# Performance work log

Hardware: AMD Instinct MI355X
Metric: run time of the kernel (lower is better)

The kernel has to match this reference:

```python
import jax, jax.numpy as jnp
import numpy as np

D_MODEL = 1024
NHEAD = 16
HEAD_DIM = D_MODEL // NHEAD


def setup_inputs() -> dict:
    key = jax.random.key(0)
    ks = jax.random.split(key, 9)
    s = 0.02
    x = jax.random.normal(ks[0], (2, 2048, D_MODEL), dtype=jnp.float32)
    Wq = jax.random.normal(ks[1], (D_MODEL, D_MODEL), dtype=jnp.float32) * s
    bq = jnp.zeros((D_MODEL,), jnp.float32)
    Wk = jax.random.normal(ks[2], (D_MODEL, D_MODEL), dtype=jnp.float32) * s
    bk = jnp.zeros((D_MODEL,), jnp.float32)
    Wv = jax.random.normal(ks[3], (D_MODEL, D_MODEL), dtype=jnp.float32) * s
    bv = jnp.zeros((D_MODEL,), jnp.float32)
    Wo = jax.random.normal(ks[4], (D_MODEL, D_MODEL), dtype=jnp.float32) * s
    bo = jnp.zeros((D_MODEL,), jnp.float32)
    return {"x": x, "Wq": Wq, "bq": bq, "Wk": Wk, "bk": bk,
            "Wv": Wv, "bv": bv, "Wo": Wo, "bo": bo}


def _rope(x, sin, cos):
    # x: [B, L, H, Dh]; rotate-half as in the torch module
    half = x.shape[-1] // 2
    x1, x2 = x[..., :half], x[..., half:]
    rotated = jnp.concatenate([-x2, x1], axis=-1)
    return x * cos + rotated * sin


def reference(x, Wq, bq, Wk, bk, Wv, bv, Wo, bo):
    B, L, D = x.shape
    H, Dh = NHEAD, HEAD_DIM
    q = (x @ Wq.T + bq).reshape(B, L, H, Dh)
    k = (x @ Wk.T + bk).reshape(B, L, H, Dh)
    v = (x @ Wv.T + bv).reshape(B, L, H, Dh)

    inv_freq = 1.0 / (10000.0 ** (jnp.arange(0, Dh, 2, dtype=jnp.float32) / Dh))
    t = jnp.arange(L, dtype=jnp.float32)
    freqs = jnp.einsum('i,j->ij', t, inv_freq)          # [L, Dh/2]
    emb = jnp.concatenate([freqs, freqs], axis=-1)      # [L, Dh]
    cos = jnp.cos(emb)[None, :, None, :]
    sin = jnp.sin(emb)[None, :, None, :]

    q = _rope(q, sin, cos)
    k = _rope(k, sin, cos)

    # [B, H, L, L]
    scores = jnp.einsum('bqhd,bkhd->bhqk', q, k) / jnp.sqrt(jnp.float32(Dh))
    attn = jax.nn.softmax(scores, axis=-1)
    # dropout in eval mode = identity (p given as 0.0)
    out = jnp.einsum('bhqk,bkhd->bqhd', attn, v).reshape(B, L, D)
    return out @ Wo.T + bo
```

## Files before the change

### kernel.cpp

```cpp
#include <hip/hip_runtime.h>
#include <math.h>

#define D_MODEL 1024
#define NHEAD 16
#define HEAD_DIM 64
#define L_SEQ 2048
#define BATCH 2
#define M_ROWS 4096
#define SC_Q 0.18033688011112042f

typedef __attribute__((ext_vector_type(8))) short short8;
typedef __attribute__((ext_vector_type(4))) float floatx4;
typedef __attribute__((ext_vector_type(2))) __fp16 half2_t;
typedef __attribute__((ext_vector_type(4))) __fp16 half4_t;

#if __has_builtin(__builtin_amdgcn_exp2f)
#define EXP2F(x) __builtin_amdgcn_exp2f(x)
#else
#define EXP2F(x) exp2f(x)
#endif

__device__ inline unsigned f2bf_u(float x) {
    unsigned u = __float_as_uint(x);
    return (u + 0x7fffu + ((u >> 16) & 1u)) >> 16;
}

__device__ inline void gl_lds16(const void* g, void* l) {
    __builtin_amdgcn_global_load_lds((const __attribute__((address_space(1))) void*)g,
                                     (__attribute__((address_space(3))) void*)l, 16, 0, 0);
}

__global__ __launch_bounds__(256) void cvt_all(
    const float* __restrict__ x,  const float* __restrict__ wq,
    const float* __restrict__ wk, const float* __restrict__ wv,
    const float* __restrict__ wo,
    unsigned short* __restrict__ xb,  unsigned short* __restrict__ wqb,
    unsigned short* __restrict__ wkb, unsigned short* __restrict__ wvb,
    unsigned short* __restrict__ wob, float* __restrict__ rt) {
    if (blockIdx.y == 5) {
        for (int idx = blockIdx.x * 256 + threadIdx.x; idx < L_SEQ * 16;
             idx += gridDim.x * 256) {
            int l = idx >> 4, f = idx & 15;
            float if0 = (float)pow(10000.0, -(double)f / 32.0);
            float if1 = (float)pow(10000.0, -(double)(f + 16) / 32.0);
            float s0, c0, s1, c1;
            sincosf((float)l * if0, &s0, &c0);
            sincosf((float)l * if1, &s1, &c1);
            float4 v = {c0, c1, s0, s1};
            *(float4*)(rt + (size_t)idx * 4) = v;
        }
        return;
    }
    const float* s; unsigned short* d; int n;
    switch (blockIdx.y) {
        case 0:  s = x;  d = xb;  n = M_ROWS * D_MODEL; break;
        case 1:  s = wq; d = wqb; n = D_MODEL * D_MODEL; break;
        case 2:  s = wk; d = wkb; n = D_MODEL * D_MODEL; break;
        case 3:  s = wv; d = wvb; n = D_MODEL * D_MODEL; break;
        default: s = wo; d = wob; n = D_MODEL * D_MODEL; break;
    }
    int stride = gridDim.x * 256 * 4;
    for (int i = (blockIdx.x * 256 + threadIdx.x) * 4; i < n; i += stride) {
        float4 v = *(const float4*)(s + i);
        ushort4 o;
        o.x = (unsigned short)f2bf_u(v.x);
        o.y = (unsigned short)f2bf_u(v.y);
        o.z = (unsigned short)f2bf_u(v.z);
        o.w = (unsigned short)f2bf_u(v.w);
        *(ushort4*)(d + i) = o;
    }
}

__global__ __launch_bounds__(256) void gemm_qkv(
    const unsigned short* __restrict__ xb,
    const unsigned short* __restrict__ wqb, const unsigned short* __restrict__ wkb,
    const unsigned short* __restrict__ wvb,
    const float* __restrict__ bq, const float* __restrict__ bk,
    const float* __restrict__ bv, const float* __restrict__ rt,
    unsigned short* __restrict__ qo, unsigned short* __restrict__ ko,
    unsigned short* __restrict__ vo) {
    __shared__ __align__(16) unsigned short As[128 * 32];
    __shared__ __align__(16) unsigned short Bs[128 * 32];

    const int K = D_MODEL;
    const int tid = threadIdx.x;
    const int lane = tid & 63;
    const int w = tid >> 6;
    const int wm = (w & 1) * 64;
    const int wn = (w >> 1) * 64;
    const int m0 = blockIdx.x * 128;
    const int n0 = blockIdx.y * 128;

    const unsigned short* Wsel; const float* bsel;
    unsigned short* osel; int mode; float oscale;
    if (blockIdx.z == 0)      { Wsel = wqb; bsel = bq; osel = qo; mode = 1; oscale = SC_Q; }
    else if (blockIdx.z == 1) { Wsel = wkb; bsel = bk; osel = ko; mode = 1; oscale = 1.0f; }
    else                      { Wsel = wvb; bsel = bv; osel = vo; mode = 2; oscale = 1.0f; }

    floatx4 acc[4][4];
#pragma unroll
    for (int i = 0; i < 4; ++i)
#pragma unroll
        for (int j = 0; j < 4; ++j) acc[i][j] = (floatx4){0.f, 0.f, 0.f, 0.f};

    const int sr = lane >> 2;
    const int ss = lane & 3;
    const unsigned short* Ag = xb + (size_t)m0 * K;
    const unsigned short* Bg = Wsel + (size_t)n0 * K;

    for (int k0 = 0; k0 < K; k0 += 32) {
        __syncthreads();
#pragma unroll
        for (int t = 0; t < 2; ++t) {
            int R0 = t * 64 + w * 16;
            int r = R0 + sr;
            int c = ss ^ ((r >> 1) & 3);
            gl_lds16(Ag + (size_t)r * K + k0 + c * 8, (void*)(As + R0 * 32));
            gl_lds16(Bg + (size_t)r * K + k0 + c * 8, (void*)(Bs + R0 * 32));
        }
        __syncthreads();

        short8 af[4], bf[4];
#pragma unroll
        for (int mt = 0; mt < 4; ++mt) {
            int ar = wm + mt * 16 + (lane & 15);
            int slot = (lane >> 4) ^ ((ar >> 1) & 3);
            af[mt] = *(const short8*)(As + ar * 32 + slot * 8);
        }
#pragma unroll
        for (int nt = 0; nt < 4; ++nt) {
            int br = wn + nt * 16 + (lane & 15);
            int slot = (lane >> 4) ^ ((br >> 1) & 3);
            bf[nt] = *(const short8*)(Bs + br * 32 + slot * 8);
        }
#pragma unroll
        for (int mt = 0; mt < 4; ++mt)
#pragma unroll
            for (int nt = 0; nt < 4; ++nt)
                acc[mt][nt] = __builtin_amdgcn_mfma_f32_16x16x32_bf16(
                    af[mt], bf[nt], acc[mt][nt], 0, 0, 0);
    }

#pragma unroll
    for (int nt = 0; nt < 4; ++nt) {
        float bn = bsel[n0 + wn + nt * 16 + (lane & 15)];
#pragma unroll
        for (int mt = 0; mt < 4; ++mt)
#pragma unroll
            for (int i = 0; i < 4; ++i) acc[mt][nt][i] += bn;
    }

    const int h = (n0 + wn) >> 6;

    if (mode == 1) {
#pragma unroll
        for (int mt = 0; mt < 4; ++mt)
#pragma unroll
            for (int i = 0; i < 4; ++i) {
                int m = m0 + wm + mt * 16 + (lane >> 4) * 4 + i;
                int b = m >> 11, l = m & (L_SEQ - 1);
                float4 tc = *(const float4*)(rt + ((size_t)(l * 16 + (lane & 15)) << 2));
#pragma unroll
                for (int nt = 0; nt < 4; ++nt) {
                    int dh = nt * 16 + (lane & 15);
                    float partner = acc[mt][nt ^ 2][i];
                    float rot = (nt < 2) ? -partner : partner;
                    float c = (nt & 1) ? tc.y : tc.x;
                    float s = (nt & 1) ? tc.w : tc.z;
                    float val = (acc[mt][nt][i] * c + rot * s) * oscale;
                    size_t idx = (((size_t)(b * NHEAD + h)) * L_SEQ + l) * HEAD_DIM + dh;
                    osel[idx] = (unsigned short)f2bf_u(val);
                }
            }
    } else {
#pragma unroll
        for (int mt = 0; mt < 4; ++mt)
#pragma unroll
            for (int ih = 0; ih < 4; ih += 2) {
                int m = m0 + wm + mt * 16 + (lane >> 4) * 4 + ih;
                int b = m >> 11, l = m & (L_SEQ - 1);
#pragma unroll
                for (int nt = 0; nt < 4; ++nt) {
                    int dh = nt * 16 + (lane & 15);
                    union { half2_t h; unsigned u; } cv;
                    cv.h = __builtin_amdgcn_cvt_pkrtz(acc[mt][nt][ih], acc[mt][nt][ih + 1]);
                    size_t idx = (((size_t)(b * NHEAD + h)) * HEAD_DIM + dh) * L_SEQ + l;
                    *(unsigned*)(vo + idx) = cv.u;
                }
            }
    }
}

__global__ __launch_bounds__(256) void gemm_out(
    const unsigned short* __restrict__ A, const unsigned short* __restrict__ Wb,
    const float* __restrict__ bias, float* __restrict__ out) {
    __shared__ __align__(16) unsigned short As[64 * 32];
    __shared__ __align__(16) unsigned short Bs[128 * 32];

    const int K = D_MODEL;
    const int tid = threadIdx.x;
    const int lane = tid & 63;
    const int w = tid >> 6;
    const int wm = (w & 1) * 32;
    const int wn = (w >> 1) * 64;
    const int m0 = blockIdx.x * 64;
    const int n0 = blockIdx.y * 128;

    floatx4 acc[2][4];
#pragma unroll
    for (int i = 0; i < 2; ++i)
#pragma unroll
        for (int j = 0; j < 4; ++j) acc[i][j] = (floatx4){0.f, 0.f, 0.f, 0.f};

    const int sr = lane >> 2;
    const int ss = lane & 3;
    const unsigned short* Ag = A + (size_t)m0 * K;
    const unsigned short* Bg = Wb + (size_t)n0 * K;

    for (int k0 = 0; k0 < K; k0 += 32) {
        __syncthreads();
        {
            int r = w * 16 + sr;
            int c = ss ^ ((r >> 1) & 3);
            gl_lds16(Ag + (size_t)r * K + k0 + c * 8, (void*)(As + (w * 16) * 32));
        }
#pragma unroll
        for (int t = 0; t < 2; ++t) {
            int R0 = t * 64 + w * 16;
            int r = R0 + sr;
            int c = ss ^ ((r >> 1) & 3);
            gl_lds16(Bg + (size_t)r * K + k0 + c * 8, (void*)(Bs + R0 * 32));
        }
        __syncthreads();

        short8 af[2], bf[4];
#pragma unroll
        for (int mt = 0; mt < 2; ++mt) {
            int ar = wm + mt * 16 + (lane & 15);
            int slot = (lane >> 4) ^ ((ar >> 1) & 3);
            af[mt] = *(const short8*)(As + ar * 32 + slot * 8);
        }
#pragma unroll
        for (int nt = 0; nt < 4; ++nt) {
            int br = wn + nt * 16 + (lane & 15);
            int slot = (lane >> 4) ^ ((br >> 1) & 3);
            bf[nt] = *(const short8*)(Bs + br * 32 + slot * 8);
        }
#pragma unroll
        for (int mt = 0; mt < 2; ++mt)
#pragma unroll
            for (int nt = 0; nt < 4; ++nt)
                acc[mt][nt] = __builtin_amdgcn_mfma_f32_16x16x32_bf16(
                    af[mt], bf[nt], acc[mt][nt], 0, 0, 0);
    }

#pragma unroll
    for (int nt = 0; nt < 4; ++nt) {
        int n = n0 + wn + nt * 16 + (lane & 15);
        float bn = bias[n];
#pragma unroll
        for (int mt = 0; mt < 2; ++mt)
#pragma unroll
            for (int i = 0; i < 4; ++i) {
                int m = m0 + wm + mt * 16 + (lane >> 4) * 4 + i;
                out[(size_t)m * D_MODEL + n] = acc[mt][nt][i] + bn;
            }
    }
}

template <int NZ>
__global__ __launch_bounds__(256, 4) void attn_mfma(
    const unsigned short* __restrict__ q, const unsigned short* __restrict__ k,
    const unsigned short* __restrict__ vt,
    float* __restrict__ opart, float* __restrict__ lpart,
    unsigned short* __restrict__ ao) {
    __shared__ __align__(16) unsigned short Ks[128 * 64];
    __shared__ __align__(16) unsigned short Vs[64 * 128];

    const int tid = threadIdx.x;
    const int lane = tid & 63;
    const int w = tid >> 6;
    const int quad = lane >> 4;
    const int ln = lane & 15;
    const int bh = blockIdx.y;
    const int q0 = blockIdx.x * 128;
    const int z = blockIdx.z;
    const int kvbase = z * (L_SEQ / NZ);

    const unsigned short* qb = q + (size_t)bh * L_SEQ * HEAD_DIM;
    const unsigned short* kb = k + (size_t)bh * L_SEQ * HEAD_DIM;
    const unsigned short* vb = vt + (size_t)bh * HEAD_DIM * L_SEQ;

    short8 qf[2][2];
#pragma unroll
    for (int ntq = 0; ntq < 2; ++ntq)
#pragma unroll
        for (int ks = 0; ks < 2; ++ks)
            qf[ntq][ks] = *(const short8*)(
                qb + (size_t)(q0 + w * 32 + ntq * 16 + ln) * HEAD_DIM
                + ks * 32 + quad * 8);

    floatx4 o[2][4];
    floatx4 ls[2];
#pragma unroll
    for (int ntq = 0; ntq < 2; ++ntq) {
        ls[ntq] = (floatx4){0.f, 0.f, 0.f, 0.f};
#pragma unroll
        for (int j = 0; j < 4; ++j) o[ntq][j] = (floatx4){0.f, 0.f, 0.f, 0.f};
    }

    half4_t ones;
#pragma unroll
    for (int j = 0; j < 4; ++j) ones[j] = (__fp16)1.0f;

    const int srk = lane >> 3;
    const int ssk = lane & 7;
    const int srv = lane >> 4;
    const int ssv = lane & 15;

    for (int t = 0; t < L_SEQ / (128 * NZ); ++t) {
        int kv0 = kvbase + t * 128;
        __syncthreads();
#pragma unroll
        for (int tt = 0; tt < 4; ++tt) {
            {
                int R0 = tt * 32 + w * 8;
                int r = R0 + srk;
                int c = ssk ^ (r & 7);
                gl_lds16(kb + (size_t)(kv0 + r) * HEAD_DIM + c * 8, (void*)(Ks + R0 * 64));
            }
            {
                int R0 = tt * 16 + w * 4;
                int r = R0 + srv;
                int c = ssv ^ (r & 15);
                gl_lds16(vb + (size_t)r * L_SEQ + kv0 + c * 8, (void*)(Vs + R0 * 128));
            }
        }
        __syncthreads();

#pragma unroll
        for (int mt = 0; mt < 8; ++mt) {
            int ar = mt * 16 + ln;
            short8 kf0 = *(const short8*)(Ks + ar * 64 + ((quad) ^ (ar & 7)) * 8);
            short8 kf1 = *(const short8*)(Ks + ar * 64 + ((4 + quad) ^ (ar & 7)) * 8);

            floatx4 s0 = (floatx4){0.f, 0.f, 0.f, 0.f};
            floatx4 s1 = (floatx4){0.f, 0.f, 0.f, 0.f};
            s0 = __builtin_amdgcn_mfma_f32_16x16x32_bf16(kf0, qf[0][0], s0, 0, 0, 0);
            s0 = __builtin_amdgcn_mfma_f32_16x16x32_bf16(kf1, qf[0][1], s0, 0, 0, 0);
            s1 = __builtin_amdgcn_mfma_f32_16x16x32_bf16(kf0, qf[1][0], s1, 0, 0, 0);
            s1 = __builtin_amdgcn_mfma_f32_16x16x32_bf16(kf1, qf[1][1], s1, 0, 0, 0);

            half4_t vf[4];
#pragma unroll
            for (int ntd = 0; ntd < 4; ++ntd) {
                int row = ntd * 16 + ln;
                int slot = (mt * 2 + (quad >> 1)) ^ ln;
                vf[ntd] = *(const half4_t*)(Vs + row * 128 + slot * 8 + (quad & 1) * 4);
            }

            {
                half2_t lo = __builtin_amdgcn_cvt_pkrtz(EXP2F(s0[0]), EXP2F(s0[1]));
                half2_t hi = __builtin_amdgcn_cvt_pkrtz(EXP2F(s0[2]), EXP2F(s0[3]));
                half4_t af; af.lo = lo; af.hi = hi;
                ls[0] = __builtin_amdgcn_mfma_f32_16x16x16f16(af, ones, ls[0], 0, 0, 0);
#pragma unroll
                for (int ntd = 0; ntd < 4; ++ntd)
                    o[0][ntd] = __builtin_amdgcn_mfma_f32_16x16x16f16(af, vf[ntd], o[0][ntd], 0, 0, 0);
            }
            {
                half2_t lo = __builtin_amdgcn_cvt_pkrtz(EXP2F(s1[0]), EXP2F(s1[1]));
                half2_t hi = __builtin_amdgcn_cvt_pkrtz(EXP2F(s1[2]), EXP2F(s1[3]));
                half4_t af; af.lo = lo; af.hi = hi;
                ls[1] = __builtin_amdgcn_mfma_f32_16x16x16f16(af, ones, ls[1], 0, 0, 0);
#pragma unroll
                for (int ntd = 0; ntd < 4; ++ntd)
                    o[1][ntd] = __builtin_amdgcn_mfma_f32_16x16x16f16(af, vf[ntd], o[1][ntd], 0, 0, 0);
            }
        }
    }

    if (NZ == 1) {
        const int b = bh >> 4, h = bh & (NHEAD - 1);
#pragma unroll
        for (int ntq = 0; ntq < 2; ++ntq)
#pragma unroll
            for (int i = 0; i < 4; ++i) {
                int l = q0 + w * 32 + ntq * 16 + quad * 4 + i;
                float inv = 1.0f / ls[ntq][i];
#pragma unroll
                for (int ntd = 0; ntd < 4; ++ntd) {
                    int dh = ntd * 16 + ln;
                    size_t idx = ((size_t)b * L_SEQ + l) * D_MODEL + h * HEAD_DIM + dh;
                    ao[idx] = (unsigned short)f2bf_u(o[ntq][ntd][i] * inv);
                }
            }
    } else {
        const size_t base = ((size_t)z * (BATCH * NHEAD) + bh) * L_SEQ;
#pragma unroll
        for (int ntq = 0; ntq < 2; ++ntq)
#pragma unroll
            for (int i = 0; i < 4; ++i) {
                int l = q0 + w * 32 + ntq * 16 + quad * 4 + i;
#pragma unroll
                for (int ntd = 0; ntd < 4; ++ntd) {
                    int dh = ntd * 16 + ln;
                    opart[(base + l) * HEAD_DIM + dh] = o[ntq][ntd][i];
                }
            }
        if (ln == 0) {
#pragma unroll
            for (int ntq = 0; ntq < 2; ++ntq)
#pragma unroll
                for (int i = 0; i < 4; ++i) {
                    int l = q0 + w * 32 + ntq * 16 + quad * 4 + i;
                    lpart[base + l] = ls[ntq][i];
                }
        }
    }
}

__global__ __launch_bounds__(256) void attn_combine(
    const float* __restrict__ opart, const float* __restrict__ lpart,
    unsigned short* __restrict__ ao) {
    const size_t R = (size_t)BATCH * NHEAD * L_SEQ;
    int e = blockIdx.x * 256 + threadIdx.x;
    int r = e >> 4;
    int dh0 = (e & 15) * 4;
    float4 a = *(const float4*)(opart + (size_t)r * HEAD_DIM + dh0);
    float4 c = *(const float4*)(opart + (R + r) * HEAD_DIM + dh0);
    float inv = 1.0f / (lpart[r] + lpart[R + r]);
    int bh = r >> 11, l = r & (L_SEQ - 1);
    int b = bh >> 4, h = bh & (NHEAD - 1);
    ushort4 ov;
    ov.x = (unsigned short)f2bf_u((a.x + c.x) * inv);
    ov.y = (unsigned short)f2bf_u((a.y + c.y) * inv);
    ov.z = (unsigned short)f2bf_u((a.z + c.z) * inv);
    ov.w = (unsigned short)f2bf_u((a.w + c.w) * inv);
    *(ushort4*)(ao + ((size_t)b * L_SEQ + l) * D_MODEL + h * HEAD_DIM + dh0) = ov;
}

extern "C" void kernel_launch(void* const* d_in, const int* in_sizes, int n_in,
                              void* d_out, int out_size, void* d_ws, size_t ws_size,
                              hipStream_t stream) {
    const float* x  = (const float*)d_in[0];
    const float* Wq = (const float*)d_in[1];
    const float* bq = (const float*)d_in[2];
    const float* Wk = (const float*)d_in[3];
    const float* bk = (const float*)d_in[4];
    const float* Wv = (const float*)d_in[5];
    const float* bv = (const float*)d_in[6];
    const float* Wo = (const float*)d_in[7];
    const float* bo = (const float*)d_in[8];
    float* outp = (float*)d_out;

    const size_t XE = (size_t)M_ROWS * D_MODEL;
    const size_t WE = (size_t)D_MODEL * D_MODEL;
    unsigned short* wqb = (unsigned short*)d_ws;
    unsigned short* wkb = wqb + WE;
    unsigned short* wvb = wkb + WE;
    unsigned short* wob = wvb + WE;
    unsigned short* qbf = wob + WE;
    unsigned short* kbf = qbf + XE;
    unsigned short* vtb = kbf + XE;
    unsigned short* xb  = vtb + XE;
    unsigned short* aob = xb;
    float* rt    = (float*)(xb + XE);
    float* lpart = rt;
    float* opart = rt + 131072;

    const size_t base_bytes  = (4 * WE + 4 * XE) * 2 + 131072 * 4;
    const size_t split_bytes = base_bytes + (size_t)8 * 1024 * 1024 * 4;
    const bool use_split = ws_size >= split_bytes;

    cvt_all<<<dim3(1024, 6), 256, 0, stream>>>(x, Wq, Wk, Wv, Wo,
                                               xb, wqb, wkb, wvb, wob, rt);

    gemm_qkv<<<dim3(M_ROWS / 128, D_MODEL / 128, 3), 256, 0, stream>>>(
        xb, wqb, wkb, wvb, bq, bk, bv, rt, qbf, kbf, vtb);

    if (use_split) {
        attn_mfma<2><<<dim3(L_SEQ / 128, BATCH * NHEAD, 2), 256, 0, stream>>>(
            qbf, kbf, vtb, opart, lpart, nullptr);
        attn_combine<<<dim3(4096), 256, 0, stream>>>(opart, lpart, aob);
    } else {
        attn_mfma<1><<<dim3(L_SEQ / 128, BATCH * NHEAD, 1), 256, 0, stream>>>(
            qbf, kbf, vtb, nullptr, nullptr, aob);
    }

    gemm_out<<<dim3(M_ROWS / 64, D_MODEL / 128), 256, 0, stream>>>(aob, wob, bo, outp);
}
```

Baseline: 197.8 us.

## Use 16x16x32 f16 MFMA for PV via permlane16_swap fragment reshuffle

The attention inner loop now processes two 16-key score tiles at once. It uses v_permlane16_swap to rearrange the exponentiated scores into the 8-element A-fragment layout of the 16x16x32 f16 MFMA. This halves the number of PV and row-sum MFMA instructions and makes V LDS reads 16-byte wide instead of 8-byte. In exchange it adds cross-lane permute instructions, raises register pressure from holding two score tiles, and relies on a gfx950-specific permlane instruction.

```diff
diff --git a/kernel.cpp b/kernel.cpp
--- a/kernel.cpp
+++ b/kernel.cpp
@@ -13,6 +13,7 @@
 typedef __attribute__((ext_vector_type(4))) float floatx4;
 typedef __attribute__((ext_vector_type(2))) __fp16 half2_t;
 typedef __attribute__((ext_vector_type(4))) __fp16 half4_t;
+typedef __attribute__((ext_vector_type(8))) __fp16 half8_t;
 
 #if __has_builtin(__builtin_amdgcn_exp2f)
 #define EXP2F(x) __builtin_amdgcn_exp2f(x)
@@ -28,6 +29,16 @@
 __device__ inline void gl_lds16(const void* g, void* l) {
     __builtin_amdgcn_global_load_lds((const __attribute__((address_space(1))) void*)g,
                                      (__attribute__((address_space(3))) void*)l, 16, 0, 0);
+}
+
+__device__ inline void permlane16_swap(unsigned& a, unsigned& b) {
+#if __has_builtin(__builtin_amdgcn_permlane16_swap)
+    auto r = __builtin_amdgcn_permlane16_swap(a, b, false, false);
+    a = r[0];
+    b = r[1];
+#else
+    asm("v_permlane16_swap_b32 %0, %1" : "+v"(a), "+v"(b));
+#endif
 }
 
 __global__ __launch_bounds__(256) void cvt_all(
@@ -309,14 +320,15 @@
         for (int j = 0; j < 4; ++j) o[ntq][j] = (floatx4){0.f, 0.f, 0.f, 0.f};
     }
 
-    half4_t ones;
-#pragma unroll
-    for (int j = 0; j < 4; ++j) ones[j] = (__fp16)1.0f;
+    half8_t ones8;
+#pragma unroll
+    for (int j = 0; j < 8; ++j) ones8[j] = (__fp16)1.0f;
 
     const int srk = lane >> 3;
     const int ssk = lane & 7;
     const int srv = lane >> 4;
     const int ssv = lane & 15;
+    const int pb = ((quad & 1) << 1) | (quad >> 1);
 
     for (int t = 0; t < L_SEQ / (128 * NZ); ++t) {
         int kv0 = kvbase + t * 128;
@@ -339,43 +351,51 @@
         __syncthreads();
 
 #pragma unroll
-        for (int mt = 0; mt < 8; ++mt) {
-            int ar = mt * 16 + ln;
-            short8 kf0 = *(const short8*)(Ks + ar * 64 + ((quad) ^ (ar & 7)) * 8);
-            short8 kf1 = *(const short8*)(Ks + ar * 64 + ((4 + quad) ^ (ar & 7)) * 8);
-
-            floatx4 s0 = (floatx4){0.f, 0.f, 0.f, 0.f};
-            floatx4 s1 = (floatx4){0.f, 0.f, 0.f, 0.f};
-            s0 = __builtin_amdgcn_mfma_f32_16x16x32_bf16(kf0, qf[0][0], s0, 0, 0, 0);
-            s0 = __builtin_amdgcn_mfma_f32_16x16x32_bf16(kf1, qf[0][1], s0, 0, 0, 0);
-            s1 = __builtin_amdgcn_mfma_f32_16x16x32_bf16(kf0, qf[1][0], s1, 0, 0, 0);
-            s1 = __builtin_amdgcn_mfma_f32_16x16x32_bf16(kf1, qf[1][1], s1, 0, 0, 0);
-
-            half4_t vf[4];
+        for (int mt2 = 0; mt2 < 4; ++mt2) {
+            floatx4 s[2][2];
+#pragma unroll
+            for (int c = 0; c < 2; ++c) {
+                int ar = mt2 * 32 + c * 16 + ln;
+                short8 kf0 = *(const short8*)(Ks + ar * 64 + ((quad) ^ (ar & 7)) * 8);
+                short8 kf1 = *(const short8*)(Ks + ar * 64 + ((4 + quad) ^ (ar & 7)) * 8);
+
+                floatx4 t0 = (floatx4){0.f, 0.f, 0.f, 0.f};
+                floatx4 t1 = (floatx4){0.f, 0.f, 0.f, 0.f};
+                t0 = __builtin_amdgcn_mfma_f32_16x16x32_bf16(kf0, qf[0][0], t0, 0, 0, 0);
+                t0 = __builtin_amdgcn_mfma_f32_16x16x32_bf16(kf1, qf[0][1], t0, 0, 0, 0);
+                t1 = __builtin_amdgcn_mfma_f32_16x16x32_bf16(kf0, qf[1][0], t1, 0, 0, 0);
+                t1 = __builtin_amdgcn_mfma_f32_16x16x32_bf16(kf1, qf[1][1], t1, 0, 0, 0);
+                s[c][0] = t0;
+                s[c][1] = t1;
+            }
+
+            half8_t vf[4];
 #pragma unroll
             for (int ntd = 0; ntd < 4; ++ntd) {
                 int row = ntd * 16 + ln;
-                int slot = (mt * 2 + (quad >> 1)) ^ ln;
-                vf[ntd] = *(const half4_t*)(Vs + row * 128 + slot * 8 + (quad & 1) * 4);
-            }
-
-            {
-                half2_t lo = __builtin_amdgcn_cvt_pkrtz(EXP2F(s0[0]), EXP2F(s0[1]));
-                half2_t hi = __builtin_amdgcn_cvt_pkrtz(EXP2F(s0[2]), EXP2F(s0[3]));
-                half4_t af; af.lo = lo; af.hi = hi;
-                ls[0] = __builtin_amdgcn_mfma_f32_16x16x16f16(af, ones, ls[0], 0, 0, 0);
+                int slot = (mt2 * 4 + pb) ^ (row & 15);
+                vf[ntd] = *(const half8_t*)(Vs + row * 128 + slot * 8);
+            }
+
+#pragma unroll
+            for (int tq = 0; tq < 2; ++tq) {
+                union { half2_t h; unsigned u; } c0l, c0h, c1l, c1h;
+                c0l.h = __builtin_amdgcn_cvt_pkrtz(EXP2F(s[0][tq][0]), EXP2F(s[0][tq][1]));
+                c0h.h = __builtin_amdgcn_cvt_pkrtz(EXP2F(s[0][tq][2]), EXP2F(s[0][tq][3]));
+                c1l.h = __builtin_amdgcn_cvt_pkrtz(EXP2F(s[1][tq][0]), EXP2F(s[1][tq][1]));
+                c1h.h = __builtin_amdgcn_cvt_pkrtz(EXP2F(s[1][tq][2]), EXP2F(s[1][tq][3]));
+                unsigned a0 = c0l.u, b0 = c1l.u;
+                unsigned a1 = c0h.u, b1 = c1h.u;
+                permlane16_swap(a0, b0);
+                permlane16_swap(a1, b1);
+                union { half8_t h8; unsigned u[4]; } af;
+                af.u[0] = a0; af.u[1] = a1; af.u[2] = b0; af.u[3] = b1;
+
+                ls[tq] = __builtin_amdgcn_mfma_f32_16x16x32_f16(af.h8, ones8, ls[tq], 0, 0, 0);
 #pragma unroll
                 for (int ntd = 0; ntd < 4; ++ntd)
-                    o[0][ntd] = __builtin_amdgcn_mfma_f32_16x16x16f16(af, vf[ntd], o[0][ntd], 0, 0, 0);
-            }
-            {
-                half2_t lo = __builtin_amdgcn_cvt_pkrtz(EXP2F(s1[0]), EXP2F(s1[1]));
-                half2_t hi = __builtin_amdgcn_cvt_pkrtz(EXP2F(s1[2]), EXP2F(s1[3]));
-                half4_t af; af.lo = lo; af.hi = hi;
-                ls[1] = __builtin_amdgcn_mfma_f32_16x16x16f16(af, ones, ls[1], 0, 0, 0);
-#pragma unroll
-                for (int ntd = 0; ntd < 4; ++ntd)
-                    o[1][ntd] = __builtin_amdgcn_mfma_f32_16x16x16f16(af, vf[ntd], o[1][ntd], 0, 0, 0);
+                    o[tq][ntd] = __builtin_amdgcn_mfma_f32_16x16x32_f16(
+                        af.h8, vf[ntd], o[tq][ntd], 0, 0, 0);
             }
         }
     }
```

After: 197.5 us. Within noise of the previous version (-0.1%).
